# Optimization experiments

Hardware: AMD Instinct MI355X
Metric: run time of the kernel (lower is better)

## Reference

```python
import jax, jax.numpy as jnp
import numpy as np

NUM_CLASSES = 1000
FEATURE_DIM = 1024
BATCH = 8192
MOMENTUM = 0.9
LAMBDA_INTRA = 1.0
LAMBDA_INTER = 0.5


def setup_inputs() -> dict:
    key = jax.random.key(0)
    k1, k2, k3, k4 = jax.random.split(key, 4)
    return {
        "features": jax.random.normal(k1, (BATCH, FEATURE_DIM), jnp.float32),
        "features_adv": jax.random.normal(k2, (BATCH, FEATURE_DIM), jnp.float32),
        "centers": jax.random.normal(k3, (NUM_CLASSES, FEATURE_DIM), jnp.float32),
        "labels": jax.random.randint(k4, (BATCH,), 0, NUM_CLASSES, dtype=jnp.int64),
    }


def _l2_normalize(x):
    # torch F.normalize(p=2, dim=1) with eps=1e-12 clamp on the norm
    n = jnp.linalg.norm(x, axis=1, keepdims=True)
    return x / jnp.maximum(n, 1e-12)


def _update_centers(centers, feats, labels):
    # Vectorized version of the per-class masked-mean momentum update.
    C = centers.shape[0]
    sums = jax.ops.segment_sum(feats, labels, num_segments=C)            # [C, D]
    counts = jax.ops.segment_sum(jnp.ones((feats.shape[0],), feats.dtype), labels, num_segments=C)  # [C]
    means = sums / jnp.maximum(counts, 1.0)[:, None]
    has_samples = (counts > 0)[:, None]
    center_is_zero = jnp.all(centers == 0, axis=1, keepdims=True)
    updated = jnp.where(center_is_zero, means, MOMENTUM * centers + (1.0 - MOMENTUM) * means)
    return jnp.where(has_samples, updated, centers)


def reference(features, features_adv, centers, labels):
    f = _l2_normalize(features)
    fa = _l2_normalize(features_adv)

    # update_centers runs under no_grad on detached normalized features
    centers_new = _update_centers(centers, jax.lax.stop_gradient(f), labels)

    centers_batch = centers_new[labels]  # [B, D] gather
    intra_clean = jnp.linalg.norm(f - centers_batch, axis=1).mean()
    intra_adv = jnp.linalg.norm(fa - centers_batch, axis=1).mean()

    # fused pairwise center distances: ||ci||^2 + ||cj||^2 - 2 ci.cj
    sq = jnp.sum(centers_new * centers_new, axis=1)                      # [C]
    d2 = sq[:, None] + sq[None, :] - 2.0 * (centers_new @ centers_new.T)  # [C, C]
    dist = jnp.sqrt(jnp.maximum(d2, 0.0))
    C = centers_new.shape[0]
    upper = jnp.triu(jnp.ones((C, C), dtype=bool), k=1)
    n_pairs = C * (C - 1) / 2.0
    inter_loss = jnp.sum(jnp.where(upper, jax.nn.relu(1.0 - dist), 0.0)) / n_pairs

    return LAMBDA_INTRA * (intra_clean + intra_adv) - LAMBDA_INTER * inter_loss
```

## Files before the change

kernel.cpp:

```cpp
#include <hip/hip_runtime.h>
#include <math.h>

#define BATCH 8192
#define DIM 1024
#define NCLS 1000
#define NPAD 1024
#define NPAIRS 499500.0f
#define INTER_TILES 136
#define MAXROWS 192

typedef float  f32x4  __attribute__((ext_vector_type(4)));
typedef short  bf16x8 __attribute__((ext_vector_type(8)));


__device__ inline float waveAllReduceAdd(float x) {
  #pragma unroll
  for (int m = 32; m > 0; m >>= 1) x += __shfl_xor(x, m);
  return x;
}

__device__ inline float blockReduce1(float x, float* sm) {
  x = waveAllReduceAdd(x);
  int lane = threadIdx.x & 63, wid = threadIdx.x >> 6;
  __syncthreads();
  if (lane == 0) sm[wid] = x;
  __syncthreads();
  return sm[0] + sm[1] + sm[2] + sm[3];
}

__device__ inline unsigned short f2bf(float f) {
  unsigned int u = __float_as_uint(f);
  u += 0x7FFFu + ((u >> 16) & 1u);
  return (unsigned short)(u >> 16);
}


__global__ __launch_bounds__(256, 4)
void update_centers_intra_kernel(const float* __restrict__ feats,
                                 const float* __restrict__ featsa,
                                 const float* __restrict__ centers,
                                 const int* __restrict__ labels,
                                 unsigned short* __restrict__ centers_bf,
                                 float* __restrict__ sqn,
                                 float* __restrict__ pclean,
                                 float* __restrict__ padv) {
  __shared__ float sm[8];
  __shared__ int s_rows[MAXROWS];
  __shared__ float s_iw[MAXROWS];
  __shared__ int s_cnt;
  __shared__ int s_anynz;
  __shared__ float4 s_acc[4][256];
  __shared__ float4 s_c[256];
  int c = blockIdx.x;
  int tid = threadIdx.x;
  int lane = tid & 63, w = tid >> 6;
  int fi = tid;

  if (c >= NCLS) {
    ((ushort4*)(centers_bf + (size_t)c * DIM))[fi] = make_ushort4(0, 0, 0, 0);
    return;
  }

  if (tid == 0) { s_cnt = 0; s_anynz = 0; }
  __syncthreads();
  #pragma unroll 4
  for (int j = tid; j < BATCH; j += 256) {
    if (labels[j] == c) {
      int p = atomicAdd(&s_cnt, 1);
      if (p < MAXROWS) s_rows[p] = j;
    }
  }
  __syncthreads();
  int n = min(s_cnt, MAXROWS);

  float4 acc[4];
  #pragma unroll
  for (int i = 0; i < 4; ++i) acc[i] = make_float4(0.f, 0.f, 0.f, 0.f);

  for (int t = w; t < n; t += 4) {
    int r = s_rows[t];
    const float4* rp = (const float4*)(feats + (size_t)r * DIM);
    float4 v[4];
    #pragma unroll
    for (int i = 0; i < 4; ++i) v[i] = rp[lane + 64 * i];
    float ss = 0.f;
    #pragma unroll
    for (int i = 0; i < 4; ++i)
      ss += v[i].x * v[i].x + v[i].y * v[i].y + v[i].z * v[i].z + v[i].w * v[i].w;
    ss = waveAllReduceAdd(ss);
    float iw = 1.0f / fmaxf(sqrtf(ss), 1e-12f);
    if (lane == 0) s_iw[t] = iw;
    #pragma unroll
    for (int i = 0; i < 4; ++i) {
      acc[i].x += v[i].x * iw; acc[i].y += v[i].y * iw;
      acc[i].z += v[i].z * iw; acc[i].w += v[i].w * iw;
    }
  }

  #pragma unroll
  for (int i = 0; i < 4; ++i) s_acc[w][lane + 64 * i] = acc[i];
  float4 cv = ((const float4*)(centers + (size_t)c * DIM))[fi];
  if (cv.x != 0.f || cv.y != 0.f || cv.z != 0.f || cv.w != 0.f) s_anynz = 1;
  __syncthreads();
  float4 a0 = s_acc[0][fi], a1 = s_acc[1][fi], a2 = s_acc[2][fi], a3 = s_acc[3][fi];
  float4 sum = make_float4(a0.x + a1.x + a2.x + a3.x, a0.y + a1.y + a2.y + a3.y,
                           a0.z + a1.z + a2.z + a3.z, a0.w + a1.w + a2.w + a3.w);

  float invc = 1.0f / fmaxf((float)n, 1.0f);
  float4 mean = make_float4(sum.x * invc, sum.y * invc, sum.z * invc, sum.w * invc);

  float4 o;
  if (s_anynz) {
    o = make_float4(0.9f * cv.x + 0.1f * mean.x, 0.9f * cv.y + 0.1f * mean.y,
                    0.9f * cv.z + 0.1f * mean.z, 0.9f * cv.w + 0.1f * mean.w);
  } else {
    o = mean;
  }
  if (n == 0) o = cv;

  ((ushort4*)(centers_bf + (size_t)c * DIM))[fi] =
      make_ushort4(f2bf(o.x), f2bf(o.y), f2bf(o.z), f2bf(o.w));
  s_c[fi] = o;

  float sq = blockReduce1(o.x * o.x + o.y * o.y + o.z * o.z + o.w * o.w, sm);
  if (tid == 0) sqn[c] = sq;
  __syncthreads();

  float sumc = 0.f;
  for (int t = w; t < n; t += 4) {
    int r = s_rows[t];
    const float4* rp = (const float4*)(feats + (size_t)r * DIM);
    float dot = 0.f;
    #pragma unroll
    for (int i = 0; i < 4; ++i) {
      float4 v = rp[lane + 64 * i];
      float4 cc = s_c[lane + 64 * i];
      dot += v.x * cc.x + v.y * cc.y + v.z * cc.z + v.w * cc.w;
    }
    dot = waveAllReduceAdd(dot);
    if (lane == 0) {
      float d2 = 1.0f + sq - 2.0f * s_iw[t] * dot;
      sumc += sqrtf(fmaxf(d2, 0.0f));
    }
  }

  float suma = 0.f;
  for (int t = w; t < n; t += 4) {
    int r = s_rows[t];
    const float4* ap = (const float4*)(featsa + (size_t)r * DIM);
    float dot = 0.f, ssa = 0.f;
    #pragma unroll
    for (int i = 0; i < 4; ++i) {
      float4 v = ap[lane + 64 * i];
      float4 cc = s_c[lane + 64 * i];
      dot += v.x * cc.x + v.y * cc.y + v.z * cc.z + v.w * cc.w;
      ssa += v.x * v.x + v.y * v.y + v.z * v.z + v.w * v.w;
    }
    dot = waveAllReduceAdd(dot);
    ssa = waveAllReduceAdd(ssa);
    if (lane == 0) {
      float inva = 1.0f / fmaxf(sqrtf(ssa), 1e-12f);
      float d2 = 1.0f + sq - 2.0f * inva * dot;
      suma += sqrtf(fmaxf(d2, 0.0f));
    }
  }

  float totc = blockReduce1(sumc, sm);
  float tota = blockReduce1(suma, sm);
  if (tid == 0) { pclean[c] = totc; padv[c] = tota; }
}


__global__ __launch_bounds__(256, 4)
void inter_mfma_kernel(const unsigned short* __restrict__ Cbf,
                       const float* __restrict__ sq,
                       float* __restrict__ pinter) {
  __shared__ float smr[8];
  int tid = threadIdx.x;
  int bid = blockIdx.x;

  int t = bid;
  int bi = 0;
  while (t >= 16 - bi) { t -= 16 - bi; ++bi; }
  int bj = bi + t;

  int w = tid >> 6;
  int wy = w >> 1, wx = w & 1;
  int lane = tid & 63;
  int m = lane & 15;
  int q = lane >> 4;

  int i0 = bi * 64 + wy * 32;
  int j0 = bj * 64 + wx * 32;

  const unsigned short* arow0 = Cbf + (size_t)(i0 + m) * DIM;
  const unsigned short* arow1 = Cbf + (size_t)(i0 + 16 + m) * DIM;
  const unsigned short* brow0 = Cbf + (size_t)(j0 + m) * DIM;
  const unsigned short* brow1 = Cbf + (size_t)(j0 + 16 + m) * DIM;

  f32x4 acc00 = {0.f, 0.f, 0.f, 0.f}, acc01 = acc00, acc10 = acc00, acc11 = acc00;

  #pragma unroll 4
  for (int k0 = 0; k0 < DIM; k0 += 32) {
    int ko = k0 + q * 8;
    bf16x8 a0 = *(const bf16x8*)(arow0 + ko);
    bf16x8 a1 = *(const bf16x8*)(arow1 + ko);
    bf16x8 b0 = *(const bf16x8*)(brow0 + ko);
    bf16x8 b1 = *(const bf16x8*)(brow1 + ko);
    acc00 = __builtin_amdgcn_mfma_f32_16x16x32_bf16(a0, b0, acc00, 0, 0, 0);
    acc01 = __builtin_amdgcn_mfma_f32_16x16x32_bf16(a0, b1, acc01, 0, 0, 0);
    acc10 = __builtin_amdgcn_mfma_f32_16x16x32_bf16(a1, b0, acc10, 0, 0, 0);
    acc11 = __builtin_amdgcn_mfma_f32_16x16x32_bf16(a1, b1, acc11, 0, 0, 0);
  }

  float local = 0.f;
  int colA = lane & 15;
  int rbase = (lane >> 4) * 4;
  #pragma unroll
  for (int si = 0; si < 2; ++si) {
    #pragma unroll
    for (int sj = 0; sj < 2; ++sj) {
      f32x4 a = (si == 0) ? (sj == 0 ? acc00 : acc01) : (sj == 0 ? acc10 : acc11);
      #pragma unroll
      for (int r = 0; r < 4; ++r) {
        int i = i0 + si * 16 + rbase + r;
        int j = j0 + sj * 16 + colA;
        if (j < NCLS && i < j) {
          float d2 = sq[i] + sq[j] - 2.0f * a[r];
          float d = sqrtf(fmaxf(d2, 0.0f));
          local += fmaxf(1.0f - d, 0.0f);
        }
      }
    }
  }
  float tot = blockReduce1(local, smr);
  if (tid == 0) pinter[bid] = tot;
}


__global__ void final_kernel(const float* __restrict__ pclean,
                             const float* __restrict__ padv,
                             const float* __restrict__ pinter,
                             float* __restrict__ out) {
  __shared__ float sm[8];
  int t = threadIdx.x;
  float ci = 0.f;
  for (int i = t; i < NCLS; i += 256) ci += pclean[i] + padv[i];
  float e = (t < INTER_TILES) ? pinter[t] : 0.f;
  ci = blockReduce1(ci, sm);
  e = blockReduce1(e, sm);
  if (t == 0) {
    float intra = ci * (1.0f / (float)BATCH);
    float inter = e / NPAIRS;
    out[0] = intra - 0.5f * inter;
  }
}


extern "C" void kernel_launch(void* const* d_in, const int* in_sizes, int n_in,
                              void* d_out, int out_size, void* d_ws, size_t ws_size,
                              hipStream_t stream) {
  const float* features     = (const float*)d_in[0];
  const float* features_adv = (const float*)d_in[1];
  const float* centers      = (const float*)d_in[2];
  const int*   labels       = (const int*)d_in[3];
  float* out = (float*)d_out;

  unsigned short* centers_bf = (unsigned short*)d_ws;
  float* sqn = (float*)(centers_bf + (size_t)NPAD * DIM);
  float* pclean = sqn + 1024;
  float* padv = pclean + 1024;
  float* pinter = padv + 1024;

  hipLaunchKernelGGL(update_centers_intra_kernel, dim3(NPAD), dim3(256), 0, stream,
                     features, features_adv, centers, labels, centers_bf, sqn,
                     pclean, padv);
  hipLaunchKernelGGL(inter_mfma_kernel, dim3(INTER_TILES), dim3(256), 0, stream,
                     centers_bf, sqn, pinter);
  hipLaunchKernelGGL(final_kernel, dim3(1), dim3(256), 0, stream, pclean, padv,
                     pinter, out);
}
```

Measured before the change: 139.7 us.

## Precompute row inverse norms in separate kernel and fuse clean/adv distance loops

Adds a kernel that computes the inverse L2 norm of every feature and adversarial row with full-grid parallelism. The per-class kernel then reads these norms instead of reducing them itself, unrolls the accumulation loop by two rows for more memory-level parallelism, and merges the clean and adversarial distance passes into one loop. The aim is to shorten the serial per-block work and cut wave reductions. The cost is an extra full read of both feature matrices (about 64 MB) plus one more kernel launch.

```diff
diff --git a/kernel.cpp b/kernel.cpp
--- a/kernel.cpp
+++ b/kernel.cpp
@@ -36,17 +36,38 @@
 
 
 __global__ __launch_bounds__(256, 4)
+void norms_kernel(const float* __restrict__ feats, const float* __restrict__ featsa,
+                  float* __restrict__ invn, float* __restrict__ invna) {
+  int lane = threadIdx.x & 63;
+  int u = blockIdx.x * 4 + (threadIdx.x >> 6);
+  int row = u >> 1;
+  const float* src = (u & 1) ? featsa : feats;
+  float* dst = (u & 1) ? invna : invn;
+  const float4* rp = (const float4*)(src + (size_t)row * DIM);
+  float ss = 0.f;
+  #pragma unroll
+  for (int i = 0; i < 4; ++i) {
+    float4 v = rp[lane + 64 * i];
+    ss += v.x * v.x + v.y * v.y + v.z * v.z + v.w * v.w;
+  }
+  ss = waveAllReduceAdd(ss);
+  if (lane == 0) dst[row] = 1.0f / fmaxf(sqrtf(ss), 1e-12f);
+}
+
+
+__global__ __launch_bounds__(256, 4)
 void update_centers_intra_kernel(const float* __restrict__ feats,
                                  const float* __restrict__ featsa,
                                  const float* __restrict__ centers,
                                  const int* __restrict__ labels,
+                                 const float* __restrict__ invn,
+                                 const float* __restrict__ invna,
                                  unsigned short* __restrict__ centers_bf,
                                  float* __restrict__ sqn,
                                  float* __restrict__ pclean,
                                  float* __restrict__ padv) {
   __shared__ float sm[8];
   __shared__ int s_rows[MAXROWS];
-  __shared__ float s_iw[MAXROWS];
   __shared__ int s_cnt;
   __shared__ int s_anynz;
   __shared__ float4 s_acc[4][256];
@@ -77,23 +98,32 @@
   #pragma unroll
   for (int i = 0; i < 4; ++i) acc[i] = make_float4(0.f, 0.f, 0.f, 0.f);
 
-  for (int t = w; t < n; t += 4) {
-    int r = s_rows[t];
-    const float4* rp = (const float4*)(feats + (size_t)r * DIM);
-    float4 v[4];
-    #pragma unroll
-    for (int i = 0; i < 4; ++i) v[i] = rp[lane + 64 * i];
-    float ss = 0.f;
-    #pragma unroll
-    for (int i = 0; i < 4; ++i)
-      ss += v[i].x * v[i].x + v[i].y * v[i].y + v[i].z * v[i].z + v[i].w * v[i].w;
-    ss = waveAllReduceAdd(ss);
-    float iw = 1.0f / fmaxf(sqrtf(ss), 1e-12f);
-    if (lane == 0) s_iw[t] = iw;
+  int t = w;
+  for (; t + 4 < n; t += 8) {
+    int r0 = s_rows[t], r1 = s_rows[t + 4];
+    float iw0 = invn[r0], iw1 = invn[r1];
+    const float4* p0 = (const float4*)(feats + (size_t)r0 * DIM);
+    const float4* p1 = (const float4*)(feats + (size_t)r1 * DIM);
+    float4 v0[4], v1[4];
+    #pragma unroll
+    for (int i = 0; i < 4; ++i) { v0[i] = p0[lane + 64 * i]; v1[i] = p1[lane + 64 * i]; }
     #pragma unroll
     for (int i = 0; i < 4; ++i) {
-      acc[i].x += v[i].x * iw; acc[i].y += v[i].y * iw;
-      acc[i].z += v[i].z * iw; acc[i].w += v[i].w * iw;
+      acc[i].x += v0[i].x * iw0 + v1[i].x * iw1;
+      acc[i].y += v0[i].y * iw0 + v1[i].y * iw1;
+      acc[i].z += v0[i].z * iw0 + v1[i].z * iw1;
+      acc[i].w += v0[i].w * iw0 + v1[i].w * iw1;
+    }
+  }
+  if (t < n) {
+    int r0 = s_rows[t];
+    float iw0 = invn[r0];
+    const float4* p0 = (const float4*)(feats + (size_t)r0 * DIM);
+    #pragma unroll
+    for (int i = 0; i < 4; ++i) {
+      float4 v = p0[lane + 64 * i];
+      acc[i].x += v.x * iw0; acc[i].y += v.y * iw0;
+      acc[i].z += v.z * iw0; acc[i].w += v.w * iw0;
     }
   }
 
@@ -126,42 +156,27 @@
   if (tid == 0) sqn[c] = sq;
   __syncthreads();
 
-  float sumc = 0.f;
-  for (int t = w; t < n; t += 4) {
-    int r = s_rows[t];
+  float sumc = 0.f, suma = 0.f;
+  for (int t2 = w; t2 < n; t2 += 4) {
+    int r = s_rows[t2];
     const float4* rp = (const float4*)(feats + (size_t)r * DIM);
-    float dot = 0.f;
+    const float4* ap = (const float4*)(featsa + (size_t)r * DIM);
+    float dotf = 0.f, dota = 0.f;
     #pragma unroll
     for (int i = 0; i < 4; ++i) {
-      float4 v = rp[lane + 64 * i];
+      float4 vf = rp[lane + 64 * i];
+      float4 va = ap[lane + 64 * i];
       float4 cc = s_c[lane + 64 * i];
-      dot += v.x * cc.x + v.y * cc.y + v.z * cc.z + v.w * cc.w;
-    }
-    dot = waveAllReduceAdd(dot);
+      dotf += vf.x * cc.x + vf.y * cc.y + vf.z * cc.z + vf.w * cc.w;
+      dota += va.x * cc.x + va.y * cc.y + va.z * cc.z + va.w * cc.w;
+    }
+    dotf = waveAllReduceAdd(dotf);
+    dota = waveAllReduceAdd(dota);
     if (lane == 0) {
-      float d2 = 1.0f + sq - 2.0f * s_iw[t] * dot;
-      sumc += sqrtf(fmaxf(d2, 0.0f));
-    }
-  }
-
-  float suma = 0.f;
-  for (int t = w; t < n; t += 4) {
-    int r = s_rows[t];
-    const float4* ap = (const float4*)(featsa + (size_t)r * DIM);
-    float dot = 0.f, ssa = 0.f;
-    #pragma unroll
-    for (int i = 0; i < 4; ++i) {
-      float4 v = ap[lane + 64 * i];
-      float4 cc = s_c[lane + 64 * i];
-      dot += v.x * cc.x + v.y * cc.y + v.z * cc.z + v.w * cc.w;
-      ssa += v.x * v.x + v.y * v.y + v.z * v.z + v.w * v.w;
-    }
-    dot = waveAllReduceAdd(dot);
-    ssa = waveAllReduceAdd(ssa);
-    if (lane == 0) {
-      float inva = 1.0f / fmaxf(sqrtf(ssa), 1e-12f);
-      float d2 = 1.0f + sq - 2.0f * inva * dot;
-      suma += sqrtf(fmaxf(d2, 0.0f));
+      float d2c = 1.0f + sq - 2.0f * invn[r] * dotf;
+      float d2a = 1.0f + sq - 2.0f * invna[r] * dota;
+      sumc += sqrtf(fmaxf(d2c, 0.0f));
+      suma += sqrtf(fmaxf(d2a, 0.0f));
     }
   }
 
@@ -268,13 +283,17 @@
 
   unsigned short* centers_bf = (unsigned short*)d_ws;
   float* sqn = (float*)(centers_bf + (size_t)NPAD * DIM);
-  float* pclean = sqn + 1024;
+  float* invn = sqn + 1024;
+  float* invna = invn + BATCH;
+  float* pclean = invna + BATCH;
   float* padv = pclean + 1024;
   float* pinter = padv + 1024;
 
+  hipLaunchKernelGGL(norms_kernel, dim3(4096), dim3(256), 0, stream,
+                     features, features_adv, invn, invna);
   hipLaunchKernelGGL(update_centers_intra_kernel, dim3(NPAD), dim3(256), 0, stream,
-                     features, features_adv, centers, labels, centers_bf, sqn,
-                     pclean, padv);
+                     features, features_adv, centers, labels, invn, invna,
+                     centers_bf, sqn, pclean, padv);
   hipLaunchKernelGGL(inter_mfma_kernel, dim3(INTER_TILES), dim3(256), 0, stream,
                      centers_bf, sqn, pinter);
   hipLaunchKernelGGL(final_kernel, dim3(1), dim3(256), 0, stream, pclean, padv,
```

Measured after the change: 148.2 us. 6.0% more time.

## Stage per-class feature rows into LDS via global_load_lds with block-wide reductions

Applied to the files above, without the earlier changes.

Rewrites the per-class center/intra kernel to fetch groups of gathered feature rows straight into shared memory with global_load_lds. Each row is then processed by the whole block, with batched block reductions in place of per-wave row ownership. The clean and adversarial distance passes are merged into one staged loop with a single 12-way reduction. This trades more __syncthreads per row group for async DMA-style loads, and lowers MAXROWS to 96, which risks truncating classes that have more than 96 samples.

```diff
diff --git a/kernel.cpp b/kernel.cpp
--- a/kernel.cpp
+++ b/kernel.cpp
@@ -7,7 +7,8 @@
 #define NPAD 1024
 #define NPAIRS 499500.0f
 #define INTER_TILES 136
-#define MAXROWS 192
+#define MAXROWS 96
+#define NSTAGE 8
 
 typedef float  f32x4  __attribute__((ext_vector_type(4)));
 typedef short  bf16x8 __attribute__((ext_vector_type(8)));
@@ -28,29 +29,56 @@
   return sm[0] + sm[1] + sm[2] + sm[3];
 }
 
+template <int N>
+__device__ inline void blockReduceN(float* vals, float (*s_red)[4]) {
+  int lane = threadIdx.x & 63, wid = threadIdx.x >> 6;
+  #pragma unroll
+  for (int k = 0; k < N; ++k) {
+    #pragma unroll
+    for (int m = 32; m > 0; m >>= 1) vals[k] += __shfl_xor(vals[k], m);
+  }
+  __syncthreads();
+  if (lane == 0) {
+    #pragma unroll
+    for (int k = 0; k < N; ++k) s_red[k][wid] = vals[k];
+  }
+  __syncthreads();
+  #pragma unroll
+  for (int k = 0; k < N; ++k)
+    vals[k] = s_red[k][0] + s_red[k][1] + s_red[k][2] + s_red[k][3];
+}
+
 __device__ inline unsigned short f2bf(float f) {
   unsigned int u = __float_as_uint(f);
   u += 0x7FFFu + ((u >> 16) & 1u);
   return (unsigned short)(u >> 16);
 }
 
+__device__ inline void gload_lds16(const float* g, float* l) {
+  __builtin_amdgcn_global_load_lds(
+      (const __attribute__((address_space(1))) void*)g,
+      (__attribute__((address_space(3))) void*)l, 16, 0, 0);
+}
+
 
 __global__ __launch_bounds__(256, 4)
-void update_centers_intra_kernel(const float* __restrict__ feats,
-                                 const float* __restrict__ featsa,
-                                 const float* __restrict__ centers,
-                                 const int* __restrict__ labels,
-                                 unsigned short* __restrict__ centers_bf,
-                                 float* __restrict__ sqn,
-                                 float* __restrict__ pclean,
-                                 float* __restrict__ padv) {
-  __shared__ float sm[8];
-  __shared__ int s_rows[MAXROWS];
-  __shared__ float s_iw[MAXROWS];
-  __shared__ int s_cnt;
-  __shared__ int s_anynz;
-  __shared__ float4 s_acc[4][256];
-  __shared__ float4 s_c[256];
+void center_intra_kernel(const float* __restrict__ feats,
+                         const float* __restrict__ featsa,
+                         const float* __restrict__ centers,
+                         const int* __restrict__ labels,
+                         unsigned short* __restrict__ centers_bf,
+                         float* __restrict__ sqn,
+                         float* __restrict__ pclean,
+                         float* __restrict__ padv) {
+  __shared__ float  s_stage[NSTAGE][DIM];
+  __shared__ float4 s_c4[256];
+  __shared__ float  s_iw[MAXROWS];
+  __shared__ int    s_rows[MAXROWS];
+  __shared__ int    s_cnt;
+  __shared__ int    s_anynz;
+  __shared__ float  s_red[12][4];
+  __shared__ float  sm[8];
+
   int c = blockIdx.x;
   int tid = threadIdx.x;
   int lane = tid & 63, w = tid >> 6;
@@ -73,41 +101,46 @@
   __syncthreads();
   int n = min(s_cnt, MAXROWS);
 
-  float4 acc[4];
-  #pragma unroll
-  for (int i = 0; i < 4; ++i) acc[i] = make_float4(0.f, 0.f, 0.f, 0.f);
-
-  for (int t = w; t < n; t += 4) {
-    int r = s_rows[t];
-    const float4* rp = (const float4*)(feats + (size_t)r * DIM);
-    float4 v[4];
-    #pragma unroll
-    for (int i = 0; i < 4; ++i) v[i] = rp[lane + 64 * i];
-    float ss = 0.f;
-    #pragma unroll
-    for (int i = 0; i < 4; ++i)
-      ss += v[i].x * v[i].x + v[i].y * v[i].y + v[i].z * v[i].z + v[i].w * v[i].w;
-    ss = waveAllReduceAdd(ss);
-    float iw = 1.0f / fmaxf(sqrtf(ss), 1e-12f);
-    if (lane == 0) s_iw[t] = iw;
-    #pragma unroll
-    for (int i = 0; i < 4; ++i) {
-      acc[i].x += v[i].x * iw; acc[i].y += v[i].y * iw;
-      acc[i].z += v[i].z * iw; acc[i].w += v[i].w * iw;
-    }
-  }
-
-  #pragma unroll
-  for (int i = 0; i < 4; ++i) s_acc[w][lane + 64 * i] = acc[i];
+  float4 acc = make_float4(0.f, 0.f, 0.f, 0.f);
+  for (int t0 = 0; t0 < n; t0 += NSTAGE) {
+    int m = min(NSTAGE, n - t0);
+    for (int j = 0; j < m; ++j) {
+      const float* src = feats + (size_t)s_rows[t0 + j] * DIM + w * 256 + lane * 4;
+      gload_lds16(src, &s_stage[j][w * 256]);
+    }
+    __syncthreads();
+
+    float red[NSTAGE];
+    #pragma unroll
+    for (int j = 0; j < NSTAGE; ++j) red[j] = 0.f;
+    #pragma unroll
+    for (int j = 0; j < NSTAGE; ++j) {
+      if (j < m) {
+        float4 v = ((const float4*)s_stage[j])[fi];
+        red[j] = v.x * v.x + v.y * v.y + v.z * v.z + v.w * v.w;
+      }
+    }
+    blockReduceN<NSTAGE>(red, s_red);
+
+    #pragma unroll
+    for (int j = 0; j < NSTAGE; ++j) {
+      if (j < m) {
+        float iw = 1.0f / fmaxf(sqrtf(red[j]), 1e-12f);
+        if (tid == 0) s_iw[t0 + j] = iw;
+        float4 v = ((const float4*)s_stage[j])[fi];
+        acc.x += v.x * iw; acc.y += v.y * iw;
+        acc.z += v.z * iw; acc.w += v.w * iw;
+      }
+    }
+    __syncthreads();
+  }
+
+  float invc = 1.0f / fmaxf((float)n, 1.0f);
+  float4 mean = make_float4(acc.x * invc, acc.y * invc, acc.z * invc, acc.w * invc);
+
   float4 cv = ((const float4*)(centers + (size_t)c * DIM))[fi];
   if (cv.x != 0.f || cv.y != 0.f || cv.z != 0.f || cv.w != 0.f) s_anynz = 1;
   __syncthreads();
-  float4 a0 = s_acc[0][fi], a1 = s_acc[1][fi], a2 = s_acc[2][fi], a3 = s_acc[3][fi];
-  float4 sum = make_float4(a0.x + a1.x + a2.x + a3.x, a0.y + a1.y + a2.y + a3.y,
-                           a0.z + a1.z + a2.z + a3.z, a0.w + a1.w + a2.w + a3.w);
-
-  float invc = 1.0f / fmaxf((float)n, 1.0f);
-  float4 mean = make_float4(sum.x * invc, sum.y * invc, sum.z * invc, sum.w * invc);
 
   float4 o;
   if (s_anynz) {
@@ -120,54 +153,54 @@
 
   ((ushort4*)(centers_bf + (size_t)c * DIM))[fi] =
       make_ushort4(f2bf(o.x), f2bf(o.y), f2bf(o.z), f2bf(o.w));
-  s_c[fi] = o;
+  s_c4[fi] = o;
 
   float sq = blockReduce1(o.x * o.x + o.y * o.y + o.z * o.z + o.w * o.w, sm);
   if (tid == 0) sqn[c] = sq;
   __syncthreads();
 
-  float sumc = 0.f;
-  for (int t = w; t < n; t += 4) {
-    int r = s_rows[t];
-    const float4* rp = (const float4*)(feats + (size_t)r * DIM);
-    float dot = 0.f;
-    #pragma unroll
-    for (int i = 0; i < 4; ++i) {
-      float4 v = rp[lane + 64 * i];
-      float4 cc = s_c[lane + 64 * i];
-      dot += v.x * cc.x + v.y * cc.y + v.z * cc.z + v.w * cc.w;
-    }
-    dot = waveAllReduceAdd(dot);
-    if (lane == 0) {
-      float d2 = 1.0f + sq - 2.0f * s_iw[t] * dot;
-      sumc += sqrtf(fmaxf(d2, 0.0f));
-    }
-  }
-
-  float suma = 0.f;
-  for (int t = w; t < n; t += 4) {
-    int r = s_rows[t];
-    const float4* ap = (const float4*)(featsa + (size_t)r * DIM);
-    float dot = 0.f, ssa = 0.f;
-    #pragma unroll
-    for (int i = 0; i < 4; ++i) {
-      float4 v = ap[lane + 64 * i];
-      float4 cc = s_c[lane + 64 * i];
-      dot += v.x * cc.x + v.y * cc.y + v.z * cc.z + v.w * cc.w;
-      ssa += v.x * v.x + v.y * v.y + v.z * v.z + v.w * v.w;
-    }
-    dot = waveAllReduceAdd(dot);
-    ssa = waveAllReduceAdd(ssa);
-    if (lane == 0) {
-      float inva = 1.0f / fmaxf(sqrtf(ssa), 1e-12f);
-      float d2 = 1.0f + sq - 2.0f * inva * dot;
-      suma += sqrtf(fmaxf(d2, 0.0f));
-    }
-  }
-
-  float totc = blockReduce1(sumc, sm);
-  float tota = blockReduce1(suma, sm);
-  if (tid == 0) { pclean[c] = totc; padv[c] = tota; }
+  float sumc = 0.f, suma = 0.f;
+  for (int t0 = 0; t0 < n; t0 += 4) {
+    int m = min(4, n - t0);
+    for (int j = 0; j < m; ++j) {
+      int r = s_rows[t0 + j];
+      gload_lds16(feats  + (size_t)r * DIM + w * 256 + lane * 4, &s_stage[j][w * 256]);
+      gload_lds16(featsa + (size_t)r * DIM + w * 256 + lane * 4, &s_stage[4 + j][w * 256]);
+    }
+    __syncthreads();
+
+    float red[12];
+    #pragma unroll
+    for (int k = 0; k < 12; ++k) red[k] = 0.f;
+    float4 cc = s_c4[fi];
+    #pragma unroll
+    for (int j = 0; j < 4; ++j) {
+      if (j < m) {
+        float4 vf = ((const float4*)s_stage[j])[fi];
+        float4 va = ((const float4*)s_stage[4 + j])[fi];
+        red[j]     = vf.x * cc.x + vf.y * cc.y + vf.z * cc.z + vf.w * cc.w;
+        red[4 + j] = va.x * cc.x + va.y * cc.y + va.z * cc.z + va.w * cc.w;
+        red[8 + j] = va.x * va.x + va.y * va.y + va.z * va.z + va.w * va.w;
+      }
+    }
+    blockReduceN<12>(red, s_red);
+
+    float sq_b = sq;
+    #pragma unroll
+    for (int j = 0; j < 4; ++j) {
+      if (j < m) {
+        float iw = s_iw[t0 + j];
+        float d2c = 1.0f + sq_b - 2.0f * iw * red[j];
+        float inva = 1.0f / fmaxf(sqrtf(red[8 + j]), 1e-12f);
+        float d2a = 1.0f + sq_b - 2.0f * inva * red[4 + j];
+        sumc += sqrtf(fmaxf(d2c, 0.0f));
+        suma += sqrtf(fmaxf(d2a, 0.0f));
+      }
+    }
+    __syncthreads();
+  }
+
+  if (tid == 0) { pclean[c] = sumc; padv[c] = suma; }
 }
 
 
@@ -272,7 +305,7 @@
   float* padv = pclean + 1024;
   float* pinter = padv + 1024;
 
-  hipLaunchKernelGGL(update_centers_intra_kernel, dim3(NPAD), dim3(256), 0, stream,
+  hipLaunchKernelGGL(center_intra_kernel, dim3(NPAD), dim3(256), 0, stream,
                      features, features_adv, centers, labels, centers_bf, sqn,
                      pclean, padv);
   hipLaunchKernelGGL(inter_mfma_kernel, dim3(INTER_TILES), dim3(256), 0, stream,
```

New measurement: 152.8 us. +9.4%, slower.

## Stage feature rows via direct global-to-LDS loads and fuse clean/adv distance passes

Applied to the files above, without the earlier changes.

Feature rows in the per-class accumulation loop are now loaded straight into a per-wave LDS staging buffer with global_load_lds, then read back as float4. The two separate passes over clean and adversarial rows for the distance terms become one loop that loads both rows and does all three reductions together, which removes a syncthreads and one loop overhead. MAXROWS drops from 192 to 128 to offset the extra LDS staging space, which truncates classes with more than 128 samples (expected count is about 8). The staging adds a full vmcnt wait per row, so loads are not overlapped with compute.

```diff
diff --git a/kernel.cpp b/kernel.cpp
--- a/kernel.cpp
+++ b/kernel.cpp
@@ -7,7 +7,7 @@
 #define NPAD 1024
 #define NPAIRS 499500.0f
 #define INTER_TILES 136
-#define MAXROWS 192
+#define MAXROWS 128
 
 typedef float  f32x4  __attribute__((ext_vector_type(4)));
 typedef short  bf16x8 __attribute__((ext_vector_type(8)));
@@ -34,23 +34,37 @@
   return (unsigned short)(u >> 16);
 }
 
+__device__ inline void gload_lds16(const float* g, float* l) {
+  __builtin_amdgcn_global_load_lds(
+      (const __attribute__((address_space(1))) void*)g,
+      (__attribute__((address_space(3))) void*)l, 16, 0, 0);
+}
+
+__device__ inline void waitvm0() {
+  asm volatile("s_waitcnt vmcnt(0)" ::: "memory");
+}
+
+__device__ inline void cfence() { asm volatile("" ::: "memory"); }
+
 
 __global__ __launch_bounds__(256, 4)
-void update_centers_intra_kernel(const float* __restrict__ feats,
-                                 const float* __restrict__ featsa,
-                                 const float* __restrict__ centers,
-                                 const int* __restrict__ labels,
-                                 unsigned short* __restrict__ centers_bf,
-                                 float* __restrict__ sqn,
-                                 float* __restrict__ pclean,
-                                 float* __restrict__ padv) {
-  __shared__ float sm[8];
-  __shared__ int s_rows[MAXROWS];
-  __shared__ float s_iw[MAXROWS];
-  __shared__ int s_cnt;
-  __shared__ int s_anynz;
-  __shared__ float4 s_acc[4][256];
-  __shared__ float4 s_c[256];
+void center_intra_kernel(const float* __restrict__ feats,
+                         const float* __restrict__ featsa,
+                         const float* __restrict__ centers,
+                         const int* __restrict__ labels,
+                         unsigned short* __restrict__ centers_bf,
+                         float* __restrict__ sqn,
+                         float* __restrict__ pclean,
+                         float* __restrict__ padv) {
+  __shared__ float  s_stage[4][DIM];
+  __shared__ float4 s_accf[4][256];
+  __shared__ float4 s_c4[256];
+  __shared__ float  s_iw[MAXROWS];
+  __shared__ int    s_rows[MAXROWS];
+  __shared__ int    s_cnt;
+  __shared__ int    s_anynz;
+  __shared__ float  sm[8];
+
   int c = blockIdx.x;
   int tid = threadIdx.x;
   int lane = tid & 63, w = tid >> 6;
@@ -76,13 +90,18 @@
   float4 acc[4];
   #pragma unroll
   for (int i = 0; i < 4; ++i) acc[i] = make_float4(0.f, 0.f, 0.f, 0.f);
+  float* myst = s_stage[w];
 
   for (int t = w; t < n; t += 4) {
     int r = s_rows[t];
-    const float4* rp = (const float4*)(feats + (size_t)r * DIM);
+    const float* src = feats + (size_t)r * DIM;
+    #pragma unroll
+    for (int q = 0; q < 4; ++q)
+      gload_lds16(src + q * 256 + lane * 4, myst + q * 256);
+    waitvm0();
     float4 v[4];
     #pragma unroll
-    for (int i = 0; i < 4; ++i) v[i] = rp[lane + 64 * i];
+    for (int i = 0; i < 4; ++i) v[i] = ((const float4*)myst)[lane + 64 * i];
     float ss = 0.f;
     #pragma unroll
     for (int i = 0; i < 4; ++i)
@@ -95,14 +114,15 @@
       acc[i].x += v[i].x * iw; acc[i].y += v[i].y * iw;
       acc[i].z += v[i].z * iw; acc[i].w += v[i].w * iw;
     }
-  }
-
-  #pragma unroll
-  for (int i = 0; i < 4; ++i) s_acc[w][lane + 64 * i] = acc[i];
+    cfence();
+  }
+
+  #pragma unroll
+  for (int i = 0; i < 4; ++i) s_accf[w][lane + 64 * i] = acc[i];
   float4 cv = ((const float4*)(centers + (size_t)c * DIM))[fi];
   if (cv.x != 0.f || cv.y != 0.f || cv.z != 0.f || cv.w != 0.f) s_anynz = 1;
   __syncthreads();
-  float4 a0 = s_acc[0][fi], a1 = s_acc[1][fi], a2 = s_acc[2][fi], a3 = s_acc[3][fi];
+  float4 a0 = s_accf[0][fi], a1 = s_accf[1][fi], a2 = s_accf[2][fi], a3 = s_accf[3][fi];
   float4 sum = make_float4(a0.x + a1.x + a2.x + a3.x, a0.y + a1.y + a2.y + a3.y,
                            a0.z + a1.z + a2.z + a3.z, a0.w + a1.w + a2.w + a3.w);
 
@@ -120,48 +140,36 @@
 
   ((ushort4*)(centers_bf + (size_t)c * DIM))[fi] =
       make_ushort4(f2bf(o.x), f2bf(o.y), f2bf(o.z), f2bf(o.w));
-  s_c[fi] = o;
+  s_c4[fi] = o;
 
   float sq = blockReduce1(o.x * o.x + o.y * o.y + o.z * o.z + o.w * o.w, sm);
   if (tid == 0) sqn[c] = sq;
-  __syncthreads();
-
-  float sumc = 0.f;
+
+  float sumc = 0.f, suma = 0.f;
   for (int t = w; t < n; t += 4) {
     int r = s_rows[t];
-    const float4* rp = (const float4*)(feats + (size_t)r * DIM);
-    float dot = 0.f;
+    const float4* rp = (const float4*)(feats  + (size_t)r * DIM);
+    const float4* ap = (const float4*)(featsa + (size_t)r * DIM);
+    float dotf = 0.f, dota = 0.f, ssa = 0.f;
     #pragma unroll
     for (int i = 0; i < 4; ++i) {
-      float4 v = rp[lane + 64 * i];
-      float4 cc = s_c[lane + 64 * i];
-      dot += v.x * cc.x + v.y * cc.y + v.z * cc.z + v.w * cc.w;
-    }
-    dot = waveAllReduceAdd(dot);
+      float4 vf = rp[lane + 64 * i];
+      float4 va = ap[lane + 64 * i];
+      float4 cc = s_c4[lane + 64 * i];
+      dotf += vf.x * cc.x + vf.y * cc.y + vf.z * cc.z + vf.w * cc.w;
+      dota += va.x * cc.x + va.y * cc.y + va.z * cc.z + va.w * cc.w;
+      ssa  += va.x * va.x + va.y * va.y + va.z * va.z + va.w * va.w;
+    }
+    dotf = waveAllReduceAdd(dotf);
+    dota = waveAllReduceAdd(dota);
+    ssa  = waveAllReduceAdd(ssa);
     if (lane == 0) {
-      float d2 = 1.0f + sq - 2.0f * s_iw[t] * dot;
-      sumc += sqrtf(fmaxf(d2, 0.0f));
-    }
-  }
-
-  float suma = 0.f;
-  for (int t = w; t < n; t += 4) {
-    int r = s_rows[t];
-    const float4* ap = (const float4*)(featsa + (size_t)r * DIM);
-    float dot = 0.f, ssa = 0.f;
-    #pragma unroll
-    for (int i = 0; i < 4; ++i) {
-      float4 v = ap[lane + 64 * i];
-      float4 cc = s_c[lane + 64 * i];
-      dot += v.x * cc.x + v.y * cc.y + v.z * cc.z + v.w * cc.w;
-      ssa += v.x * v.x + v.y * v.y + v.z * v.z + v.w * v.w;
-    }
-    dot = waveAllReduceAdd(dot);
-    ssa = waveAllReduceAdd(ssa);
-    if (lane == 0) {
+      float iw = s_iw[t];
       float inva = 1.0f / fmaxf(sqrtf(ssa), 1e-12f);
-      float d2 = 1.0f + sq - 2.0f * inva * dot;
-      suma += sqrtf(fmaxf(d2, 0.0f));
+      float d2c = 1.0f + sq - 2.0f * iw * dotf;
+      float d2a = 1.0f + sq - 2.0f * inva * dota;
+      sumc += sqrtf(fmaxf(d2c, 0.0f));
+      suma += sqrtf(fmaxf(d2a, 0.0f));
     }
   }
 
@@ -272,7 +280,7 @@
   float* padv = pclean + 1024;
   float* pinter = padv + 1024;
 
-  hipLaunchKernelGGL(update_centers_intra_kernel, dim3(NPAD), dim3(256), 0, stream,
+  hipLaunchKernelGGL(center_intra_kernel, dim3(NPAD), dim3(256), 0, stream,
                      features, features_adv, centers, labels, centers_bf, sqn,
                      pclean, padv);
   hipLaunchKernelGGL(inter_mfma_kernel, dim3(INTER_TILES), dim3(256), 0, stream,
```

Measured after the change: 138.7 us. Within noise of the previous version (-0.7%).
